# Kernel tuning notes

Measured on AMD Instinct MI355X. Metric: run time of the kernel, lower is better.

The kernel has to match this reference:

```python
import jax, jax.numpy as jnp
import numpy as np

C, B, N, IN, OUT = 10, 128, 1152, 8, 16  # num_capsules, batch, num_route_nodes, in_ch, out_ch
NUM_ITERS = 3


def squash(t):
    # t: [..., OUT]
    sq_norm = jnp.sum(t * t, axis=-1, keepdims=True)
    scale = sq_norm / (1.0 + sq_norm)
    return scale * t / jnp.sqrt(sq_norm + 1e-8)


def setup_inputs() -> dict:
    key = jax.random.key(0)
    k1, k2 = jax.random.split(key)
    x = jax.random.normal(k1, (B, N, IN), dtype=jnp.float32)
    route_weights = jax.random.normal(k2, (C, N, IN, OUT), dtype=jnp.float32)
    return {"x": x, "route_weights": route_weights}


def reference(x, route_weights):
    # priors[c,b,n,o] = sum_i x[b,n,i] * W[c,n,i,o]
    priors = jnp.einsum('bni,cnio->cbno', x, route_weights)  # [C,B,N,OUT]
    # torch: logits = zeros_like(priors[:, :, :, 0]) -> [C,B,N,OUT] (dim 3 was the
    # singleton matmul row dim, so the OUT axis survives on the logits)
    logits = jnp.zeros_like(priors)
    outputs = None
    for _ in range(NUM_ITERS):
        attn = jax.nn.softmax(logits, axis=2)            # over route nodes N
        outputs = squash(jnp.sum(attn * priors, axis=2))  # [C,B,OUT]
        # (outputs * priors).sum(-1) broadcasts to [C,B,N,1] added to [C,B,N,OUT]
        logits = logits + jnp.sum(outputs[:, :, None, :] * priors, axis=-1, keepdims=True)
    return outputs  # [C,B,OUT] == outputs.squeeze() in torch (B>1, C>1)
```

## Files before the change

### kernel.cpp

```cpp
#include <hip/hip_runtime.h>


constexpr int C = 10, B = 128, N = 1152, IN = 8, OUT = 16;
constexpr int THREADS = 384;
constexpr int NW = THREADS / 64;
constexpr int PASSES = N / (NW * 16);

__global__ __launch_bounds__(THREADS)
void caps_route(const float* __restrict__ Xf, const float* __restrict__ Wf,
                float* __restrict__ Of) {
    __shared__ float lds_s[NW][OUT];
    __shared__ float lds_sum[NW];
    __shared__ float lds_out[OUT];

    const int t = threadIdx.x;
    const int l = t & 63;
    const int wid = t >> 6;
    const int q = l & 3;
    const int rsub = l >> 2;
    const int blk = blockIdx.x;
    const int c = blk >> 7;
    const int b = blk & 127;

    float P[PASSES][4];
    float logit[PASSES];

    #pragma unroll
    for (int p = 0; p < PASSES; ++p) {
        const int n = wid * (16 * PASSES) + p * 16 + rsub;
        const float4* wr = (const float4*)(Wf + (size_t)(c * N + n) * (IN * OUT));
        const float4* xr = (const float4*)(Xf + (size_t)(b * N + n) * IN);
        const float4 xa = xr[0], xb = xr[1];
        const float xs[8] = { xa.x, xa.y, xa.z, xa.w, xb.x, xb.y, xb.z, xb.w };
        float a0 = 0.f, a1 = 0.f, a2 = 0.f, a3 = 0.f;
        #pragma unroll
        for (int i = 0; i < IN; ++i) {
            const float4 w = wr[i * 4 + q];
            a0 = fmaf(xs[i], w.x, a0);
            a1 = fmaf(xs[i], w.y, a1);
            a2 = fmaf(xs[i], w.z, a2);
            a3 = fmaf(xs[i], w.w, a3);
        }
        P[p][0] = a0; P[p][1] = a1; P[p][2] = a2; P[p][3] = a3;
        logit[p] = 0.f;
    }

    for (int it = 0; it < 3; ++it) {
        float s0 = 0.f, s1 = 0.f, s2 = 0.f, s3 = 0.f, ssum = 0.f;
        #pragma unroll
        for (int p = 0; p < PASSES; ++p) {
            const float e = __expf(logit[p]);
            ssum += e;
            s0 = fmaf(e, P[p][0], s0);
            s1 = fmaf(e, P[p][1], s1);
            s2 = fmaf(e, P[p][2], s2);
            s3 = fmaf(e, P[p][3], s3);
        }
        #pragma unroll
        for (int m = 4; m < 64; m <<= 1) {
            ssum += __shfl_xor(ssum, m, 64);
            s0 += __shfl_xor(s0, m, 64);
            s1 += __shfl_xor(s1, m, 64);
            s2 += __shfl_xor(s2, m, 64);
            s3 += __shfl_xor(s3, m, 64);
        }
        if (l < 4) {
            lds_s[wid][l * 4 + 0] = s0;
            lds_s[wid][l * 4 + 1] = s1;
            lds_s[wid][l * 4 + 2] = s2;
            lds_s[wid][l * 4 + 3] = s3;
        }
        if (l == 0) lds_sum[wid] = ssum;
        __syncthreads();

        if (t < OUT) {
            float so = 0.f, S = 0.f;
            #pragma unroll
            for (int w = 0; w < NW; ++w) { so += lds_s[w][t]; S += lds_sum[w]; }
            so /= S;
            float r = so * so;
            r += __shfl_xor(r, 1, 64);
            r += __shfl_xor(r, 2, 64);
            r += __shfl_xor(r, 4, 64);
            r += __shfl_xor(r, 8, 64);
            const float ov = so * (r / ((1.f + r) * sqrtf(r + 1e-8f)));
            if (it == 2) Of[((size_t)c * B + b) * OUT + t] = ov;
            else         lds_out[t] = ov;
        }

        if (it < 2) {
            __syncthreads();
            const float o0 = lds_out[q * 4 + 0];
            const float o1 = lds_out[q * 4 + 1];
            const float o2 = lds_out[q * 4 + 2];
            const float o3 = lds_out[q * 4 + 3];
            #pragma unroll
            for (int p = 0; p < PASSES; ++p) {
                float d = o0 * P[p][0];
                d = fmaf(o1, P[p][1], d);
                d = fmaf(o2, P[p][2], d);
                d = fmaf(o3, P[p][3], d);
                d += __shfl_xor(d, 1, 64);
                d += __shfl_xor(d, 2, 64);
                logit[p] += d;
            }
        }
    }
}

extern "C" void kernel_launch(void* const* d_in, const int* in_sizes, int n_in,
                              void* d_out, int out_size, void* d_ws, size_t ws_size,
                              hipStream_t stream) {
    const float* X = (const float*)d_in[0];
    const float* W = (const float*)d_in[1];
    float* O = (float*)d_out;
    hipLaunchKernelGGL(caps_route, dim3(C * B), dim3(THREADS), 0, stream, X, W, O);
}
```

Baseline: 100.9 us.

## Split into priors GEMM with bf16 workspace and LDS-staged routing kernel

Measured after the change: 96.28 us. 1.05x faster.

```diff
diff --git a/kernel.cpp b/kernel.cpp
--- a/kernel.cpp
+++ b/kernel.cpp
@@ -1,16 +1,67 @@
 #include <hip/hip_runtime.h>
+#include <hip/hip_bf16.h>
 
 
 constexpr int C = 10, B = 128, N = 1152, IN = 8, OUT = 16;
-constexpr int THREADS = 384;
-constexpr int NW = THREADS / 64;
-constexpr int PASSES = N / (NW * 16);
 
-__global__ __launch_bounds__(THREADS)
-void caps_route(const float* __restrict__ Xf, const float* __restrict__ Wf,
-                float* __restrict__ Of) {
-    __shared__ float lds_s[NW][OUT];
-    __shared__ float lds_sum[NW];
+__device__ __forceinline__ unsigned packbf(float a, float b) {
+    __hip_bfloat162 h = __float22bfloat162_rn(float2{a, b});
+    return *(unsigned*)&h;
+}
+__device__ __forceinline__ float bflo(unsigned u) { return __uint_as_float(u << 16); }
+__device__ __forceinline__ float bfhi(unsigned u) { return __uint_as_float(u & 0xffff0000u); }
+
+constexpr int T1 = 512;
+constexpr int BT = 16;
+
+__global__ __launch_bounds__(T1)
+void priors_gemm(const float* __restrict__ Xf, const float* __restrict__ Wf,
+                 uint2* __restrict__ Pws) {
+    const int t = threadIdx.x;
+    const int l = t & 63;
+    const int wid = t >> 6;
+    const int q = l & 3;
+    const int rsub = l >> 2;
+    const int blk = blockIdx.x;
+    const int bt = blk & 7;
+    const int rest = blk >> 3;
+    const int nc = rest % 9;
+    const int c = rest / 9;
+    const int n = nc * 128 + wid * 16 + rsub;
+
+    const float4* wr = (const float4*)(Wf + (size_t)(c * N + n) * (IN * OUT));
+    float4 wv[IN];
+    #pragma unroll
+    for (int i = 0; i < IN; ++i) wv[i] = wr[i * 4 + q];
+
+    #pragma unroll 4
+    for (int g = 0; g < BT; ++g) {
+        const int b = bt * BT + g;
+        const float4* xr = (const float4*)(Xf + (size_t)(b * N + n) * IN);
+        const float4 xa = xr[0], xc = xr[1];
+        const float xs[8] = { xa.x, xa.y, xa.z, xa.w, xc.x, xc.y, xc.z, xc.w };
+        float a0 = 0.f, a1 = 0.f, a2 = 0.f, a3 = 0.f;
+        #pragma unroll
+        for (int i = 0; i < IN; ++i) {
+            a0 = fmaf(xs[i], wv[i].x, a0);
+            a1 = fmaf(xs[i], wv[i].y, a1);
+            a2 = fmaf(xs[i], wv[i].z, a2);
+            a3 = fmaf(xs[i], wv[i].w, a3);
+        }
+        Pws[((size_t)(c * B + b) * N + n) * 4 + q] =
+            uint2{packbf(a0, a1), packbf(a2, a3)};
+    }
+}
+
+constexpr int T2 = 512;
+constexpr int NW2 = T2 / 64;
+constexpr int PASSES = N / (NW2 * 16);
+
+__global__ __launch_bounds__(T2)
+void routing(const uint2* __restrict__ Pws, float* __restrict__ Of) {
+    __shared__ uint2 ldsP[N * 4];
+    __shared__ float lds_s[NW2][OUT];
+    __shared__ float lds_sum[NW2];
     __shared__ float lds_out[OUT];
 
     const int t = threadIdx.x;
@@ -19,42 +70,46 @@
     const int q = l & 3;
     const int rsub = l >> 2;
     const int blk = blockIdx.x;
-    const int c = blk >> 7;
-    const int b = blk & 127;
 
-    float P[PASSES][4];
-    float logit[PASSES];
+    const uint2* src = Pws + (size_t)blk * (N * 4);
+    #pragma unroll
+    for (int k = 0; k < (N * 4) / T2; ++k)
+        ldsP[k * T2 + t] = src[k * T2 + t];
+    __syncthreads();
 
-    #pragma unroll
-    for (int p = 0; p < PASSES; ++p) {
-        const int n = wid * (16 * PASSES) + p * 16 + rsub;
-        const float4* wr = (const float4*)(Wf + (size_t)(c * N + n) * (IN * OUT));
-        const float4* xr = (const float4*)(Xf + (size_t)(b * N + n) * IN);
-        const float4 xa = xr[0], xb = xr[1];
-        const float xs[8] = { xa.x, xa.y, xa.z, xa.w, xb.x, xb.y, xb.z, xb.w };
-        float a0 = 0.f, a1 = 0.f, a2 = 0.f, a3 = 0.f;
-        #pragma unroll
-        for (int i = 0; i < IN; ++i) {
-            const float4 w = wr[i * 4 + q];
-            a0 = fmaf(xs[i], w.x, a0);
-            a1 = fmaf(xs[i], w.y, a1);
-            a2 = fmaf(xs[i], w.z, a2);
-            a3 = fmaf(xs[i], w.w, a3);
-        }
-        P[p][0] = a0; P[p][1] = a1; P[p][2] = a2; P[p][3] = a3;
-        logit[p] = 0.f;
-    }
+    float oa[4] = {0.f, 0.f, 0.f, 0.f};
 
     for (int it = 0; it < 3; ++it) {
         float s0 = 0.f, s1 = 0.f, s2 = 0.f, s3 = 0.f, ssum = 0.f;
-        #pragma unroll
-        for (int p = 0; p < PASSES; ++p) {
-            const float e = __expf(logit[p]);
-            ssum += e;
-            s0 = fmaf(e, P[p][0], s0);
-            s1 = fmaf(e, P[p][1], s1);
-            s2 = fmaf(e, P[p][2], s2);
-            s3 = fmaf(e, P[p][3], s3);
+        if (it == 0) {
+            ssum = (float)PASSES;
+            #pragma unroll
+            for (int p = 0; p < PASSES; ++p) {
+                const int n = wid * (16 * PASSES) + p * 16 + rsub;
+                const uint2 u = ldsP[n * 4 + q];
+                s0 += bflo(u.x); s1 += bfhi(u.x);
+                s2 += bflo(u.y); s3 += bfhi(u.y);
+            }
+        } else {
+            #pragma unroll
+            for (int p = 0; p < PASSES; ++p) {
+                const int n = wid * (16 * PASSES) + p * 16 + rsub;
+                const uint2 u = ldsP[n * 4 + q];
+                const float p0 = bflo(u.x), p1 = bfhi(u.x);
+                const float p2 = bflo(u.y), p3 = bfhi(u.y);
+                float d = oa[0] * p0;
+                d = fmaf(oa[1], p1, d);
+                d = fmaf(oa[2], p2, d);
+                d = fmaf(oa[3], p3, d);
+                d += __shfl_xor(d, 1, 64);
+                d += __shfl_xor(d, 2, 64);
+                const float e = __expf(d);
+                ssum += e;
+                s0 = fmaf(e, p0, s0);
+                s1 = fmaf(e, p1, s1);
+                s2 = fmaf(e, p2, s2);
+                s3 = fmaf(e, p3, s3);
+            }
         }
         #pragma unroll
         for (int m = 4; m < 64; m <<= 1) {
@@ -76,7 +131,7 @@
         if (t < OUT) {
             float so = 0.f, S = 0.f;
             #pragma unroll
-            for (int w = 0; w < NW; ++w) { so += lds_s[w][t]; S += lds_sum[w]; }
+            for (int w = 0; w < NW2; ++w) { so += lds_s[w][t]; S += lds_sum[w]; }
             so /= S;
             float r = so * so;
             r += __shfl_xor(r, 1, 64);
@@ -84,26 +139,16 @@
             r += __shfl_xor(r, 4, 64);
             r += __shfl_xor(r, 8, 64);
             const float ov = so * (r / ((1.f + r) * sqrtf(r + 1e-8f)));
-            if (it == 2) Of[((size_t)c * B + b) * OUT + t] = ov;
+            if (it == 2) Of[(size_t)blk * OUT + t] = ov;
             else         lds_out[t] = ov;
         }
 
         if (it < 2) {
             __syncthreads();
-            const float o0 = lds_out[q * 4 + 0];
-            const float o1 = lds_out[q * 4 + 1];
-            const float o2 = lds_out[q * 4 + 2];
-            const float o3 = lds_out[q * 4 + 3];
-            #pragma unroll
-            for (int p = 0; p < PASSES; ++p) {
-                float d = o0 * P[p][0];
-                d = fmaf(o1, P[p][1], d);
-                d = fmaf(o2, P[p][2], d);
-                d = fmaf(o3, P[p][3], d);
-                d += __shfl_xor(d, 1, 64);
-                d += __shfl_xor(d, 2, 64);
-                logit[p] += d;
-            }
+            oa[0] += lds_out[q * 4 + 0];
+            oa[1] += lds_out[q * 4 + 1];
+            oa[2] += lds_out[q * 4 + 2];
+            oa[3] += lds_out[q * 4 + 3];
         }
     }
 }
@@ -114,5 +159,8 @@
     const float* X = (const float*)d_in[0];
     const float* W = (const float*)d_in[1];
     float* O = (float*)d_out;
-    hipLaunchKernelGGL(caps_route, dim3(C * B), dim3(THREADS), 0, stream, X, W, O);
+    uint2* P = (uint2*)d_ws;
+
+    hipLaunchKernelGGL(priors_gemm, dim3(C * 9 * 8), dim3(T1), 0, stream, X, W, P);
+    hipLaunchKernelGGL(routing, dim3(C * B), dim3(T2), 0, stream, P, O);
 }
```
